# Performance work log

Hardware: AMD Instinct MI355X
Metric: run time of the kernel (lower is better)

The kernel has to match this reference:

```python
import jax, jax.numpy as jnp
import numpy as np

D, H, KVH, HD, FF = 768, 12, 4, 64, 2048
N_REP = H // KVH
EPS = 1e-6


def rmsnorm(x, w):
    # Faithful to source: norm = ||x|| * n^{-1/2}; eps added to norm (not inside sqrt)
    norm = jnp.sqrt(jnp.sum(x * x, axis=-1, keepdims=True)) * (x.shape[-1] ** -0.5)
    return w * x / (norm + EPS)


def rope_tables(seq_len, head_dim, base=10000.0):
    inv_freq = 1.0 / (base ** (np.arange(0, head_dim, 2, dtype=np.float32) / head_dim))
    t = np.arange(seq_len, dtype=np.float32)
    freqs = np.einsum('i,j->ij', t, inv_freq)  # [S, HD/2]
    emb = np.concatenate([freqs, freqs], axis=-1)  # [S, HD]
    return jnp.asarray(np.cos(emb)), jnp.asarray(np.sin(emb))


def rotate_half(x):
    h = x.shape[-1] // 2
    return jnp.concatenate([-x[..., h:], x[..., :h]], axis=-1)


def setup_inputs() -> dict:
    key = jax.random.key(0)
    ks = jax.random.split(key, 9)
    s = 0.02
    return {
        'x': jax.random.normal(ks[0], (2, 2048, D), jnp.float32),
        'Wq': jax.random.normal(ks[1], (H * HD, D), jnp.float32) * s,
        'Wk': jax.random.normal(ks[2], (KVH * HD, D), jnp.float32) * s,
        'Wv': jax.random.normal(ks[3], (KVH * HD, D), jnp.float32) * s,
        'Wo': jax.random.normal(ks[4], (D, H * HD), jnp.float32) * s,
        'Wgate': jax.random.normal(ks[5], (FF, D), jnp.float32) * s,
        'Wup': jax.random.normal(ks[6], (FF, D), jnp.float32) * s,
        'Wdown': jax.random.normal(ks[7], (D, FF), jnp.float32) * s,
        'g1': jnp.ones((D,), jnp.float32),
        'g2': jnp.ones((D,), jnp.float32),
    }


def reference(x, Wq, Wk, Wv, Wo, Wgate, Wup, Wdown, g1, g2):
    B, S, _ = x.shape
    # ---- attention sublayer (pre-norm) ----
    xn = rmsnorm(x, g1)
    q = (xn @ Wq.T).reshape(B, S, H, HD).transpose(0, 2, 1, 3)      # [B,H,S,HD]
    k = (xn @ Wk.T).reshape(B, S, KVH, HD).transpose(0, 2, 1, 3)    # [B,KVH,S,HD]
    v = (xn @ Wv.T).reshape(B, S, KVH, HD).transpose(0, 2, 1, 3)
    cos, sin = rope_tables(S, HD)                                   # [S,HD]
    q = q * cos + rotate_half(q) * sin
    k = k * cos + rotate_half(k) * sin
    # repeat kv heads to match q heads
    k = jnp.repeat(k, N_REP, axis=1)                                # [B,H,S,HD]
    v = jnp.repeat(v, N_REP, axis=1)
    scores = jnp.einsum('bhqd,bhkd->bhqk', q, k) / jnp.sqrt(jnp.float32(HD))
    causal = jnp.tril(jnp.ones((S, S), bool))
    scores = jnp.where(causal, scores, jnp.finfo(scores.dtype).min)
    attn = jax.nn.softmax(scores, axis=-1)
    out = jnp.einsum('bhqk,bhkd->bhqd', attn, v)                    # [B,H,S,HD]
    out = out.transpose(0, 2, 1, 3).reshape(B, S, H * HD) @ Wo.T
    x = x + out
    # ---- SwiGLU FFN sublayer (pre-norm) ----
    xn2 = rmsnorm(x, g2)
    ff = (jax.nn.silu(xn2 @ Wgate.T) * (xn2 @ Wup.T)) @ Wdown.T
    return x + ff
```

## Files before the change

kernel.cpp:

```cpp
#include <hip/hip_runtime.h>
#include <hip/hip_bf16.h>
#include <math.h>

typedef __bf16 bf16;
typedef __attribute__((ext_vector_type(8))) __bf16 bf16x8;
typedef __attribute__((ext_vector_type(4))) __bf16 bf16x4;
typedef __attribute__((ext_vector_type(4))) float f32x4;

#define MFMA16(a,b,c) __builtin_amdgcn_mfma_f32_16x16x32_bf16(a,b,c,0,0,0)

#define BATCH 2
#define SEQ   2048
#define DMODEL 768
#define NH    12
#define NKV   4
#define NREP  3
#define HD    64
#define FFDIM 2048
#define ROWS  (BATCH*SEQ)

#define QSCALE 0.18033688011112042f
#define LOG2E  1.4426950408889634f

#define WB(N) asm volatile("s_waitcnt vmcnt(" #N ")\n\ts_barrier" ::: "memory")
#define BAR() asm volatile("s_barrier" ::: "memory")

__device__ __forceinline__ void gl2lds16(const bf16* g, bf16* l) {
  __builtin_amdgcn_global_load_lds(
      (const __attribute__((address_space(1))) void*)g,
      (__attribute__((address_space(3))) void*)l, 16, 0, 0);
}

struct Cvt7 { const float* s[7]; bf16* d[7]; int n[7]; };
__global__ __launch_bounds__(256) void cvt_all_kernel(Cvt7 c) {
  int seg = blockIdx.y;
  const float* __restrict__ src = c.s[seg];
  bf16* __restrict__ dst = c.d[seg];
  int n4 = c.n[seg] >> 2;
  int stride = gridDim.x * 256;
  for (int i = blockIdx.x * 256 + threadIdx.x; i < n4; i += stride) {
    f32x4 v = ((const f32x4*)src)[i];
    bf16x4 o;
    #pragma unroll
    for (int j = 0; j < 4; ++j) o[j] = (bf16)v[j];
    ((bf16x4*)dst)[i] = o;
  }
}

__global__ __launch_bounds__(256) void rope_tab_kernel(float* __restrict__ tab) {
  int id = blockIdx.x * 256 + threadIdx.x;
  int j = id >> 11, s = id & 2047;
  float inv = expf(-(float)j * (9.210340371976184f / 32.0f));
  float ang = (float)s * inv;
  tab[id] = cosf(ang);
  tab[65536 + id] = sinf(ang);
}

__global__ __launch_bounds__(192) void rmsnorm_kernel(const float* __restrict__ x,
    const float* __restrict__ g, bf16* __restrict__ out) {
  int row = blockIdx.x;
  const float* xr = x + (size_t)row * DMODEL;
  int t = threadIdx.x;
  f32x4 v = *(const f32x4*)(xr + t * 4);
  float ss = v[0] * v[0] + v[1] * v[1] + v[2] * v[2] + v[3] * v[3];
  #pragma unroll
  for (int off = 32; off; off >>= 1) ss += __shfl_xor(ss, off, 64);
  __shared__ float red[3];
  if ((t & 63) == 0) red[t >> 6] = ss;
  __syncthreads();
  float total = red[0] + red[1] + red[2];
  float norm = sqrtf(total) * 0.03608439182435161f;
  float sc = 1.0f / (norm + 1e-6f);
  f32x4 gv = *(const f32x4*)(g + t * 4);
  bf16x4 o;
  #pragma unroll
  for (int i = 0; i < 4; ++i) o[i] = (bf16)(gv[i] * v[i] * sc);
  *(bf16x4*)(out + (size_t)row * DMODEL + t * 4) = o;
}

__global__ __launch_bounds__(256) void gemm_pipe64_kernel(const bf16* __restrict__ A,
    const bf16* __restrict__ B, float* __restrict__ C, const float* __restrict__ R,
    int N, int K) {
  __shared__ __align__(16) bf16 At[4][64 * 32];
  __shared__ __align__(16) bf16 Bt[4][64 * 32];
  int t = threadIdx.x, lane = t & 63, wave = t >> 6;
  int l15 = lane & 15, lq = lane >> 4;
  int wrow = (wave >> 1) * 32, wcol = (wave & 1) * 32;
  int row0 = blockIdx.y * 64, col0 = blockIdx.x * 64;
  const bf16* Ag = A + (size_t)(row0 + (t >> 2)) * K + (t & 3) * 8;
  const bf16* Bg = B + (size_t)(col0 + (t >> 2)) * K + (t & 3) * 8;
  const int NS = K / 32;

  #pragma unroll
  for (int s = 0; s < 3; ++s) {
    int ks = s * 32;
    gl2lds16(Ag + ks, At[s] + t * 8);
    gl2lds16(Bg + ks, Bt[s] + t * 8);
  }

  f32x4 zero = {0.f, 0.f, 0.f, 0.f};
  f32x4 acc[2][2];
  #pragma unroll
  for (int m = 0; m < 2; ++m)
    #pragma unroll
    for (int n = 0; n < 2; ++n) acc[m][n] = zero;

  #define GP_COMPUTE(slot) do {                                              \
    const bf16* at = At[slot]; const bf16* bt = Bt[slot];                    \
    bf16x8 af[2], bfr[2];                                                    \
    _Pragma("unroll")                                                        \
    for (int m = 0; m < 2; ++m)                                              \
      af[m] = *(const bf16x8*)(at + (wrow + m * 16 + l15) * 32 + lq * 8);    \
    _Pragma("unroll")                                                        \
    for (int n = 0; n < 2; ++n)                                              \
      bfr[n] = *(const bf16x8*)(bt + (wcol + n * 16 + l15) * 32 + lq * 8);   \
    _Pragma("unroll")                                                        \
    for (int m = 0; m < 2; ++m)                                              \
      _Pragma("unroll")                                                      \
      for (int n = 0; n < 2; ++n)                                            \
        acc[m][n] = MFMA16(af[m], bfr[n], acc[m][n]);                        \
  } while (0)

  for (int k = 0; k < NS - 3; ++k) {
    WB(4);
    int ks = (k + 3) * 32;
    gl2lds16(Ag + ks, At[(k + 3) & 3] + t * 8);
    gl2lds16(Bg + ks, Bt[(k + 3) & 3] + t * 8);
    GP_COMPUTE(k & 3);
  }
  for (int k = NS - 3; k < NS; ++k) {
    WB(0);
    GP_COMPUTE(k & 3);
  }
  #undef GP_COMPUTE

  #pragma unroll
  for (int m = 0; m < 2; ++m)
    #pragma unroll
    for (int n = 0; n < 2; ++n)
      #pragma unroll
      for (int r = 0; r < 4; ++r) {
        size_t idx = (size_t)(row0 + wrow + m * 16 + lq * 4 + r) * N
                   + (col0 + wcol + n * 16 + l15);
        C[idx] = acc[m][n][r] + R[idx];
      }
}

__global__ __launch_bounds__(256) void gemm_qkv_kernel(const bf16* __restrict__ A,
    const bf16* __restrict__ Wcat, const float* __restrict__ tab,
    bf16* __restrict__ Qh, bf16* __restrict__ Kh, bf16* __restrict__ Vt) {
  __shared__ __align__(16) bf16 At[4][64 * 32];
  __shared__ __align__(16) bf16 Bt[4][128 * 32];
  const int K = DMODEL;
  int t = threadIdx.x, lane = t & 63, wave = t >> 6;
  int l15 = lane & 15, lq = lane >> 4;
  int wrow = (wave >> 1) * 32, wcol = (wave & 1) * 64;
  int row0 = blockIdx.y * 64, col0 = blockIdx.x * 128;
  const bf16* Ag  = A + (size_t)(row0 + (t >> 2)) * K + (t & 3) * 8;
  const bf16* Bg0 = Wcat + (size_t)(col0 + (t >> 2)) * K + (t & 3) * 8;
  const bf16* Bg1 = Bg0 + (size_t)64 * K;
  const int NS = K / 32;

  #pragma unroll
  for (int s = 0; s < 3; ++s) {
    int ks = s * 32;
    gl2lds16(Ag + ks,  At[s] + t * 8);
    gl2lds16(Bg0 + ks, Bt[s] + t * 8);
    gl2lds16(Bg1 + ks, Bt[s] + 2048 + t * 8);
  }

  f32x4 zero = {0.f, 0.f, 0.f, 0.f};
  f32x4 acc[2][4];
  #pragma unroll
  for (int m = 0; m < 2; ++m)
    #pragma unroll
    for (int n = 0; n < 4; ++n) acc[m][n] = zero;

  #define QK_COMPUTE(slot) do {                                              \
    const bf16* at = At[slot]; const bf16* bt = Bt[slot];                    \
    bf16x8 af[2], bfr[4];                                                    \
    _Pragma("unroll")                                                        \
    for (int m = 0; m < 2; ++m)                                              \
      af[m] = *(const bf16x8*)(at + (wrow + m * 16 + l15) * 32 + lq * 8);    \
    _Pragma("unroll")                                                        \
    for (int n = 0; n < 4; ++n)                                              \
      bfr[n] = *(const bf16x8*)(bt + (wcol + n * 16 + l15) * 32 + lq * 8);   \
    _Pragma("unroll")                                                        \
    for (int m = 0; m < 2; ++m)                                              \
      _Pragma("unroll")                                                      \
      for (int n = 0; n < 4; ++n)                                            \
        acc[m][n] = MFMA16(af[m], bfr[n], acc[m][n]);                        \
  } while (0)

  for (int k = 0; k < NS - 3; ++k) {
    WB(6);
    int ks = (k + 3) * 32;
    gl2lds16(Ag + ks,  At[(k + 3) & 3] + t * 8);
    gl2lds16(Bg0 + ks, Bt[(k + 3) & 3] + t * 8);
    gl2lds16(Bg1 + ks, Bt[(k + 3) & 3] + 2048 + t * 8);
    QK_COMPUTE(k & 3);
  }
  for (int k = NS - 3; k < NS; ++k) {
    WB(0);
    QK_COMPUTE(k & 3);
  }
  #undef QK_COMPUTE

  int b = row0 >> 11;
  int s0 = (row0 & 2047) + wrow + lq * 4;
  int colw = col0 + wcol;
  if (colw < 768) {
    int h = colw >> 6;
    f32x4 cv[2][2], sv[2][2];
    #pragma unroll
    for (int m = 0; m < 2; ++m)
      #pragma unroll
      for (int jh = 0; jh < 2; ++jh) {
        const float* cp = tab + (jh * 16 + l15) * 2048 + s0 + m * 16;
        cv[m][jh] = *(const f32x4*)cp;
        sv[m][jh] = *(const f32x4*)(cp + 65536);
      }
    #pragma unroll
    for (int m = 0; m < 2; ++m)
      #pragma unroll
      for (int n = 0; n < 4; ++n) {
        float sgn = (n < 2) ? -1.f : 1.f;
        #pragma unroll
        for (int r = 0; r < 4; ++r) {
          float c = cv[m][n & 1][r], si = sv[m][n & 1][r];
          float rp = (acc[m][n][r] * c + sgn * acc[m][n ^ 2][r] * si) * QSCALE;
          Qh[((size_t)(b * NH + h) * SEQ + s0 + m * 16 + r) * 64 + n * 16 + l15] = (bf16)rp;
        }
      }
  } else if (colw < 1024) {
    int kh = (colw - 768) >> 6;
    f32x4 cv[2][2], sv[2][2];
    #pragma unroll
    for (int m = 0; m < 2; ++m)
      #pragma unroll
      for (int jh = 0; jh < 2; ++jh) {
        const float* cp = tab + (jh * 16 + l15) * 2048 + s0 + m * 16;
        cv[m][jh] = *(const f32x4*)cp;
        sv[m][jh] = *(const f32x4*)(cp + 65536);
      }
    #pragma unroll
    for (int m = 0; m < 2; ++m)
      #pragma unroll
      for (int n = 0; n < 4; ++n) {
        float sgn = (n < 2) ? -1.f : 1.f;
        #pragma unroll
        for (int r = 0; r < 4; ++r) {
          float c = cv[m][n & 1][r], si = sv[m][n & 1][r];
          float rp = acc[m][n][r] * c + sgn * acc[m][n ^ 2][r] * si;
          Kh[((size_t)(b * NKV + kh) * SEQ + s0 + m * 16 + r) * 64 + n * 16 + l15] = (bf16)rp;
        }
      }
  } else {
    int vh = (colw - 1024) >> 6;
    #pragma unroll
    for (int m = 0; m < 2; ++m)
      #pragma unroll
      for (int n = 0; n < 4; ++n) {
        bf16x4 pv;
        #pragma unroll
        for (int r = 0; r < 4; ++r) pv[r] = (bf16)acc[m][n][r];
        *(bf16x4*)(Vt + ((size_t)(b * NKV + vh) * 64 + n * 16 + l15) * SEQ + s0 + m * 16) = pv;
      }
  }
}

__global__ __launch_bounds__(256, 2) void gemm_gu_kernel(const bf16* __restrict__ A,
    const bf16* __restrict__ Wg, const bf16* __restrict__ Wu, bf16* __restrict__ H) {
  __shared__ __align__(16) bf16 At[3][128 * 32];
  __shared__ __align__(16) bf16 Bgt[3][128 * 32];
  __shared__ __align__(16) bf16 But[3][128 * 32];
  const int K = DMODEL;
  int t = threadIdx.x, lane = t & 63, wave = t >> 6;
  int l15 = lane & 15, lq = lane >> 4;
  int wrow = (wave >> 1) * 64, wcol = (wave & 1) * 64;
  int row0 = blockIdx.y * 128, col0 = blockIdx.x * 128;
  const bf16* Ag0 = A + (size_t)(row0 + (t >> 2)) * K + (t & 3) * 8;
  const bf16* Ag1 = Ag0 + (size_t)64 * K;
  const bf16* Gg0 = Wg + (size_t)(col0 + (t >> 2)) * K + (t & 3) * 8;
  const bf16* Gg1 = Gg0 + (size_t)64 * K;
  const bf16* Ug0 = Wu + (size_t)(col0 + (t >> 2)) * K + (t & 3) * 8;
  const bf16* Ug1 = Ug0 + (size_t)64 * K;
  const int NS = K / 32;

  #pragma unroll
  for (int s = 0; s < 2; ++s) {
    int ks = s * 32;
    gl2lds16(Ag0 + ks, At[s] + t * 8);
    gl2lds16(Ag1 + ks, At[s] + 2048 + t * 8);
    gl2lds16(Gg0 + ks, Bgt[s] + t * 8);
    gl2lds16(Gg1 + ks, Bgt[s] + 2048 + t * 8);
    gl2lds16(Ug0 + ks, But[s] + t * 8);
    gl2lds16(Ug1 + ks, But[s] + 2048 + t * 8);
  }

  f32x4 zero = {0.f, 0.f, 0.f, 0.f};
  f32x4 ag[4][4], au[4][4];
  #pragma unroll
  for (int m = 0; m < 4; ++m)
    #pragma unroll
    for (int n = 0; n < 4; ++n) { ag[m][n] = zero; au[m][n] = zero; }

  #define GU_COMPUTE(slot) do {                                              \
    const bf16* at = At[slot];                                               \
    const bf16* bgt = Bgt[slot]; const bf16* but = But[slot];                \
    bf16x8 af[4], bg[4], bu[4];                                              \
    _Pragma("unroll")                                                        \
    for (int m = 0; m < 4; ++m)                                              \
      af[m] = *(const bf16x8*)(at + (wrow + m * 16 + l15) * 32 + lq * 8);    \
    _Pragma("unroll")                                                        \
    for (int n = 0; n < 4; ++n) {                                            \
      bg[n] = *(const bf16x8*)(bgt + (wcol + n * 16 + l15) * 32 + lq * 8);   \
      bu[n] = *(const bf16x8*)(but + (wcol + n * 16 + l15) * 32 + lq * 8);   \
    }                                                                        \
    _Pragma("unroll")                                                        \
    for (int m = 0; m < 4; ++m)                                              \
      _Pragma("unroll")                                                      \
      for (int n = 0; n < 4; ++n) {                                          \
        ag[m][n] = MFMA16(af[m], bg[n], ag[m][n]);                           \
        au[m][n] = MFMA16(af[m], bu[n], au[m][n]);                           \
      }                                                                      \
  } while (0)

  int sc = 0, sw = 2;
  for (int k = 0; k < NS - 2; ++k) {
    WB(6);
    int ks = (k + 2) * 32;
    gl2lds16(Ag0 + ks, At[sw] + t * 8);
    gl2lds16(Ag1 + ks, At[sw] + 2048 + t * 8);
    gl2lds16(Gg0 + ks, Bgt[sw] + t * 8);
    gl2lds16(Gg1 + ks, Bgt[sw] + 2048 + t * 8);
    gl2lds16(Ug0 + ks, But[sw] + t * 8);
    gl2lds16(Ug1 + ks, But[sw] + 2048 + t * 8);
    GU_COMPUTE(sc);
    sc = (sc == 2) ? 0 : sc + 1;
    sw = (sw == 2) ? 0 : sw + 1;
  }
  for (int k = NS - 2; k < NS; ++k) {
    WB(0);
    GU_COMPUTE(sc);
    sc = (sc == 2) ? 0 : sc + 1;
  }
  #undef GU_COMPUTE

  #pragma unroll
  for (int m = 0; m < 4; ++m)
    #pragma unroll
    for (int n = 0; n < 4; ++n)
      #pragma unroll
      for (int r = 0; r < 4; ++r) {
        int row = row0 + wrow + m * 16 + lq * 4 + r;
        int col = col0 + wcol + n * 16 + l15;
        float g = ag[m][n][r], u = au[m][n][r];
        float sg = g / (1.f + __builtin_amdgcn_exp2f(-g * LOG2E));
        H[(size_t)row * FFDIM + col] = (bf16)(sg * u);
      }
}

__global__ __launch_bounds__(256) void attn_kernel(const bf16* __restrict__ Qh,
    const bf16* __restrict__ Kh, const bf16* __restrict__ Vt, bf16* __restrict__ out) {
  __shared__ __align__(16) bf16 Kl0[2][64 * 32];
  __shared__ __align__(16) bf16 Kl1[2][64 * 32];
  __shared__ __align__(16) bf16 Vl0[2][64 * 32];
  __shared__ __align__(16) bf16 Vl1[2][64 * 32];
  __shared__ __align__(16) bf16 P[4][16 * 80];

  int idx = blockIdx.x;
  int qt = 31 - (idx / 24);
  int bh = idx % 24;
  int q0blk = qt * 64;
  int b = bh / NH, h = bh % NH;
  int kvh = h / NREP;
  int t = threadIdx.x;
  int lane = t & 63, wave = t >> 6;
  int l15 = lane & 15, lq = lane >> 4;
  int qw = q0blk + wave * 16;
  const bf16* Qb = Qh + (size_t)(b * NH + h) * SEQ * 64;
  const bf16* Kb = Kh + (size_t)(b * NKV + kvh) * SEQ * 64;
  const bf16* Vb = Vt + (size_t)(b * NKV + kvh) * 64 * SEQ;

  bf16x8 bq0 = *(const bf16x8*)(Qb + (size_t)(qw + l15) * 64 + lq * 8);
  bf16x8 bq1 = *(const bf16x8*)(Qb + (size_t)(qw + l15) * 64 + 32 + lq * 8);

  const bf16* Kg = Kb + (size_t)(t >> 2) * 64 + (t & 3) * 8;
  const bf16* Vg = Vb + (size_t)(t >> 2) * SEQ + (t & 3) * 8;
  bf16* Pw = P[wave];
  int Pwq = l15 * 80, lq8 = lq * 8, lq4 = lq * 4;
  const int NS = qt + 1;

  #pragma unroll
  for (int s = 0; s < 2; ++s) {
    int ks = (s < NS ? s : NS - 1) * 64;
    gl2lds16(Kg + (size_t)ks * 64,      Kl0[s] + t * 8);
    gl2lds16(Kg + (size_t)ks * 64 + 32, Kl1[s] + t * 8);
    gl2lds16(Vg + ks,                   Vl0[s] + t * 8);
    gl2lds16(Vg + ks + 32,              Vl1[s] + t * 8);
  }

  f32x4 zero = {0.f, 0.f, 0.f, 0.f};
  f32x4 o[4];
  o[0] = zero; o[1] = zero; o[2] = zero; o[3] = zero;
  float l_r = 0.f;

  #define ATTN_STEP(kk, slot) do {                                           \
    int k0 = (kk) * 64;                                                      \
    const bf16* kl0 = Kl0[slot]; const bf16* kl1 = Kl1[slot];                \
    const bf16* vl0 = Vl0[slot]; const bf16* vl1 = Vl1[slot];                \
    f32x4 s[4];                                                              \
    _Pragma("unroll")                                                        \
    for (int c = 0; c < 4; ++c) {                                            \
      bf16x8 ak0 = *(const bf16x8*)(kl0 + (c * 16 + l15) * 32 + lq8);        \
      bf16x8 ak1 = *(const bf16x8*)(kl1 + (c * 16 + l15) * 32 + lq8);        \
      s[c] = zero;                                                           \
      s[c] = MFMA16(ak0, bq0, s[c]);                                         \
      s[c] = MFMA16(ak1, bq1, s[c]);                                         \
    }                                                                        \
    if (k0 + 63 > qw) {                                                      \
      int qmk = qw + l15 - k0 - lq4;                                         \
      _Pragma("unroll")                                                      \
      for (int c = 0; c < 4; ++c)                                            \
        _Pragma("unroll")                                                    \
        for (int r = 0; r < 4; ++r)                                          \
          if (c * 16 + r > qmk) s[c][r] = -INFINITY;                         \
    }                                                                        \
    _Pragma("unroll")                                                        \
    for (int c = 0; c < 4; ++c) {                                            \
      bf16x4 pe;                                                             \
      _Pragma("unroll")                                                      \
      for (int r = 0; r < 4; ++r) {                                          \
        float e = __builtin_amdgcn_exp2f(s[c][r]);                           \
        l_r += e;                                                            \
        pe[r] = (bf16)e;                                                     \
      }                                                                      \
      *(bf16x4*)(Pw + Pwq + c * 16 + lq4) = pe;                              \
    }                                                                        \
    bf16x8 bp0 = *(const bf16x8*)(Pw + Pwq + lq8);                           \
    bf16x8 bp1 = *(const bf16x8*)(Pw + Pwq + 32 + lq8);                      \
    _Pragma("unroll")                                                        \
    for (int n = 0; n < 4; ++n) {                                            \
      bf16x8 av0 = *(const bf16x8*)(vl0 + (n * 16 + l15) * 32 + lq8);        \
      bf16x8 av1 = *(const bf16x8*)(vl1 + (n * 16 + l15) * 32 + lq8);        \
      o[n] = MFMA16(av0, bp0, o[n]);                                         \
      o[n] = MFMA16(av1, bp1, o[n]);                                         \
    }                                                                        \
  } while (0)

  for (int k = 0; k < NS - 1; ++k) {
    WB(4);
    ATTN_STEP(k, k & 1);
    BAR();
    if (k <= NS - 3) {
      int ks = (k + 2) * 64;
      gl2lds16(Kg + (size_t)ks * 64,      Kl0[k & 1] + t * 8);
      gl2lds16(Kg + (size_t)ks * 64 + 32, Kl1[k & 1] + t * 8);
      gl2lds16(Vg + ks,                   Vl0[k & 1] + t * 8);
      gl2lds16(Vg + ks + 32,              Vl1[k & 1] + t * 8);
    }
  }
  {
    WB(0);
    ATTN_STEP(NS - 1, (NS - 1) & 1);
  }
  #undef ATTN_STEP

  float lt = l_r;
  lt += __shfl_xor(lt, 16, 64);
  lt += __shfl_xor(lt, 32, 64);
  float inv = 1.f / lt;
  int q = qw + l15;
  bf16* orow = out + (size_t)(b * SEQ + q) * DMODEL + h * 64;
  #pragma unroll
  for (int n = 0; n < 4; ++n) {
    bf16x4 po;
    #pragma unroll
    for (int r = 0; r < 4; ++r) po[r] = (bf16)(o[n][r] * inv);
    *(bf16x4*)(orow + n * 16 + lq4) = po;
  }
}

extern "C" void kernel_launch(void* const* d_in, const int* in_sizes, int n_in,
                              void* d_out, int out_size, void* d_ws, size_t ws_size,
                              hipStream_t stream) {
  const float* x     = (const float*)d_in[0];
  const float* Wq    = (const float*)d_in[1];
  const float* Wk    = (const float*)d_in[2];
  const float* Wv    = (const float*)d_in[3];
  const float* Wo    = (const float*)d_in[4];
  const float* Wgate = (const float*)d_in[5];
  const float* Wup   = (const float*)d_in[6];
  const float* Wdown = (const float*)d_in[7];
  const float* g1    = (const float*)d_in[8];
  const float* g2    = (const float*)d_in[9];
  float* out = (float*)d_out;

  char* ws = (char*)d_ws;
  size_t off = 0;
  auto alloc = [&](size_t bytes) { size_t o = off; off += (bytes + 255) & ~(size_t)255; return o; };
  size_t o_tab  = alloc((size_t)2 * 32 * 2048 * 4);
  size_t o_x1   = alloc((size_t)4096 * 768 * 4);
  size_t o_xn   = alloc((size_t)4096 * 768 * 2);
  size_t o_Qh   = alloc((size_t)2 * 12 * 2048 * 64 * 2);
  size_t o_Kh   = alloc((size_t)2 * 4 * 2048 * 64 * 2);
  size_t o_Vt   = alloc((size_t)2 * 4 * 64 * 2048 * 2);
  size_t o_ao   = alloc((size_t)4096 * 768 * 2);
  size_t o_H    = alloc((size_t)4096 * 2048 * 2);
  size_t o_Wcat = alloc((size_t)1280 * 768 * 2);
  size_t o_Wo   = alloc((size_t)768 * 768 * 2);
  size_t o_Wgu  = alloc((size_t)4096 * 768 * 2);
  size_t o_Wdn  = alloc((size_t)768 * 2048 * 2);
  if (ws_size < off) return;

  float* tab  = (float*)(ws + o_tab);
  float* fx1  = (float*)(ws + o_x1);
  bf16* bxn   = (bf16*)(ws + o_xn);
  bf16* bQh   = (bf16*)(ws + o_Qh);
  bf16* bKh   = (bf16*)(ws + o_Kh);
  bf16* bVt   = (bf16*)(ws + o_Vt);
  bf16* bao   = (bf16*)(ws + o_ao);
  bf16* bH    = (bf16*)(ws + o_H);
  bf16* bWcat = (bf16*)(ws + o_Wcat);
  bf16* bWo   = (bf16*)(ws + o_Wo);
  bf16* bWgu  = (bf16*)(ws + o_Wgu);
  bf16* bWdn  = (bf16*)(ws + o_Wdn);

  rope_tab_kernel<<<256, 256, 0, stream>>>(tab);

  Cvt7 c;
  c.s[0] = Wq;    c.d[0] = bWcat;              c.n[0] = 768 * 768;
  c.s[1] = Wk;    c.d[1] = bWcat + 768 * 768;  c.n[1] = 256 * 768;
  c.s[2] = Wv;    c.d[2] = bWcat + 1024 * 768; c.n[2] = 256 * 768;
  c.s[3] = Wo;    c.d[3] = bWo;                c.n[3] = 768 * 768;
  c.s[4] = Wgate; c.d[4] = bWgu;               c.n[4] = 2048 * 768;
  c.s[5] = Wup;   c.d[5] = bWgu + 2048 * 768;  c.n[5] = 2048 * 768;
  c.s[6] = Wdown; c.d[6] = bWdn;               c.n[6] = 768 * 2048;
  cvt_all_kernel<<<dim3(256, 7), 256, 0, stream>>>(c);

  rmsnorm_kernel<<<4096, 192, 0, stream>>>(x, g1, bxn);
  gemm_qkv_kernel<<<dim3(10, 64), 256, 0, stream>>>(bxn, bWcat, tab, bQh, bKh, bVt);
  attn_kernel<<<dim3(768), 256, 0, stream>>>(bQh, bKh, bVt, bao);
  gemm_pipe64_kernel<<<dim3(12, 64), 256, 0, stream>>>(bao, bWo, fx1, x, 768, 768);

  rmsnorm_kernel<<<4096, 192, 0, stream>>>(fx1, g2, bxn);
  gemm_gu_kernel<<<dim3(16, 32), 256, 0, stream>>>(bxn, bWgu, bWgu + 2048 * 768, bH);
  gemm_pipe64_kernel<<<dim3(12, 64), 256, 0, stream>>>(bH, bWdn, out, fx1, 768, 2048);
}
```

Before: 256.6 us.

## Replace triple-buffered gate/up GEMM with single-buffered 128x64 tiles

Rewrites the fused gate/up SwiGLU GEMM to use a 128x64 output tile per block (twice as many blocks) with a single LDS buffer and two barriers per K step, instead of the 128x128 tile with three-stage async prefetch. This cuts LDS and register use per block and drops the occupancy hint, aiming to raise occupancy and grid size. In exchange it gives up overlap of global loads with MFMA compute and reloads the A tile twice as often.

```diff
diff --git a/kernel.cpp b/kernel.cpp
--- a/kernel.cpp
+++ b/kernel.cpp
@@ -269,88 +269,63 @@
   }
 }
 
-__global__ __launch_bounds__(256, 2) void gemm_gu_kernel(const bf16* __restrict__ A,
+__global__ __launch_bounds__(256) void gemm_gu_kernel(const bf16* __restrict__ A,
     const bf16* __restrict__ Wg, const bf16* __restrict__ Wu, bf16* __restrict__ H) {
-  __shared__ __align__(16) bf16 At[3][128 * 32];
-  __shared__ __align__(16) bf16 Bgt[3][128 * 32];
-  __shared__ __align__(16) bf16 But[3][128 * 32];
+  __shared__ __align__(16) bf16 At[128 * 32];
+  __shared__ __align__(16) bf16 Bgt[64 * 32];
+  __shared__ __align__(16) bf16 But[64 * 32];
   const int K = DMODEL;
-  int t = threadIdx.x, lane = t & 63, wave = t >> 6;
+  int t = threadIdx.x;
+  int lane = t & 63, wave = t >> 6;
   int l15 = lane & 15, lq = lane >> 4;
-  int wrow = (wave >> 1) * 64, wcol = (wave & 1) * 64;
-  int row0 = blockIdx.y * 128, col0 = blockIdx.x * 128;
-  const bf16* Ag0 = A + (size_t)(row0 + (t >> 2)) * K + (t & 3) * 8;
+  int wrow = (wave >> 1) * 64, wcol = (wave & 1) * 32;
+  int row0 = blockIdx.y * 128;
+  int col0 = blockIdx.x * 64;
+  int srow = t >> 2, sseg = (t & 3) * 8;
+  const bf16* Ag0 = A + (size_t)(row0 + srow) * K + sseg;
   const bf16* Ag1 = Ag0 + (size_t)64 * K;
-  const bf16* Gg0 = Wg + (size_t)(col0 + (t >> 2)) * K + (t & 3) * 8;
-  const bf16* Gg1 = Gg0 + (size_t)64 * K;
-  const bf16* Ug0 = Wu + (size_t)(col0 + (t >> 2)) * K + (t & 3) * 8;
-  const bf16* Ug1 = Ug0 + (size_t)64 * K;
-  const int NS = K / 32;
-
-  #pragma unroll
-  for (int s = 0; s < 2; ++s) {
-    int ks = s * 32;
-    gl2lds16(Ag0 + ks, At[s] + t * 8);
-    gl2lds16(Ag1 + ks, At[s] + 2048 + t * 8);
-    gl2lds16(Gg0 + ks, Bgt[s] + t * 8);
-    gl2lds16(Gg1 + ks, Bgt[s] + 2048 + t * 8);
-    gl2lds16(Ug0 + ks, But[s] + t * 8);
-    gl2lds16(Ug1 + ks, But[s] + 2048 + t * 8);
-  }
+  const bf16* Gg = Wg + (size_t)(col0 + srow) * K + sseg;
+  const bf16* Ug = Wu + (size_t)(col0 + srow) * K + sseg;
+  bf16* Al0 = At + t * 8;
+  bf16* Al1 = At + 2048 + t * 8;
+  bf16* Bgd = Bgt + t * 8;
+  bf16* Bud = But + t * 8;
 
   f32x4 zero = {0.f, 0.f, 0.f, 0.f};
-  f32x4 ag[4][4], au[4][4];
+  f32x4 ag[4][2], au[4][2];
   #pragma unroll
   for (int m = 0; m < 4; ++m)
     #pragma unroll
-    for (int n = 0; n < 4; ++n) { ag[m][n] = zero; au[m][n] = zero; }
-
-  #define GU_COMPUTE(slot) do {                                              \
-    const bf16* at = At[slot];                                               \
-    const bf16* bgt = Bgt[slot]; const bf16* but = But[slot];                \
-    bf16x8 af[4], bg[4], bu[4];                                              \
-    _Pragma("unroll")                                                        \
-    for (int m = 0; m < 4; ++m)                                              \
-      af[m] = *(const bf16x8*)(at + (wrow + m * 16 + l15) * 32 + lq * 8);    \
-    _Pragma("unroll")                                                        \
-    for (int n = 0; n < 4; ++n) {                                            \
-      bg[n] = *(const bf16x8*)(bgt + (wcol + n * 16 + l15) * 32 + lq * 8);   \
-      bu[n] = *(const bf16x8*)(but + (wcol + n * 16 + l15) * 32 + lq * 8);   \
-    }                                                                        \
-    _Pragma("unroll")                                                        \
-    for (int m = 0; m < 4; ++m)                                              \
-      _Pragma("unroll")                                                      \
-      for (int n = 0; n < 4; ++n) {                                          \
-        ag[m][n] = MFMA16(af[m], bg[n], ag[m][n]);                           \
-        au[m][n] = MFMA16(af[m], bu[n], au[m][n]);                           \
-      }                                                                      \
-  } while (0)
-
-  int sc = 0, sw = 2;
-  for (int k = 0; k < NS - 2; ++k) {
-    WB(6);
-    int ks = (k + 2) * 32;
-    gl2lds16(Ag0 + ks, At[sw] + t * 8);
-    gl2lds16(Ag1 + ks, At[sw] + 2048 + t * 8);
-    gl2lds16(Gg0 + ks, Bgt[sw] + t * 8);
-    gl2lds16(Gg1 + ks, Bgt[sw] + 2048 + t * 8);
-    gl2lds16(Ug0 + ks, But[sw] + t * 8);
-    gl2lds16(Ug1 + ks, But[sw] + 2048 + t * 8);
-    GU_COMPUTE(sc);
-    sc = (sc == 2) ? 0 : sc + 1;
-    sw = (sw == 2) ? 0 : sw + 1;
-  }
-  for (int k = NS - 2; k < NS; ++k) {
-    WB(0);
-    GU_COMPUTE(sc);
-    sc = (sc == 2) ? 0 : sc + 1;
-  }
-  #undef GU_COMPUTE
-
+    for (int n = 0; n < 2; ++n) { ag[m][n] = zero; au[m][n] = zero; }
+
+  for (int k0 = 0; k0 < K; k0 += 32) {
+    __syncthreads();
+    gl2lds16(Ag0 + k0, Al0);
+    gl2lds16(Ag1 + k0, Al1);
+    gl2lds16(Gg + k0, Bgd);
+    gl2lds16(Ug + k0, Bud);
+    __syncthreads();
+    bf16x8 af[4], bg[2], bu[2];
+    #pragma unroll
+    for (int m = 0; m < 4; ++m)
+      af[m] = *(const bf16x8*)(At + (wrow + m * 16 + l15) * 32 + lq * 8);
+    #pragma unroll
+    for (int n = 0; n < 2; ++n) {
+      bg[n] = *(const bf16x8*)(Bgt + (wcol + n * 16 + l15) * 32 + lq * 8);
+      bu[n] = *(const bf16x8*)(But + (wcol + n * 16 + l15) * 32 + lq * 8);
+    }
+    #pragma unroll
+    for (int m = 0; m < 4; ++m)
+      #pragma unroll
+      for (int n = 0; n < 2; ++n) {
+        ag[m][n] = MFMA16(af[m], bg[n], ag[m][n]);
+        au[m][n] = MFMA16(af[m], bu[n], au[m][n]);
+      }
+  }
   #pragma unroll
   for (int m = 0; m < 4; ++m)
     #pragma unroll
-    for (int n = 0; n < 4; ++n)
+    for (int n = 0; n < 2; ++n)
       #pragma unroll
       for (int r = 0; r < 4; ++r) {
         int row = row0 + wrow + m * 16 + lq * 4 + r;
@@ -545,6 +520,6 @@
   gemm_pipe64_kernel<<<dim3(12, 64), 256, 0, stream>>>(bao, bWo, fx1, x, 768, 768);
 
   rmsnorm_kernel<<<4096, 192, 0, stream>>>(fx1, g2, bxn);
-  gemm_gu_kernel<<<dim3(16, 32), 256, 0, stream>>>(bxn, bWgu, bWgu + 2048 * 768, bH);
+  gemm_gu_kernel<<<dim3(32, 32), 256, 0, stream>>>(bxn, bWgu, bWgu + 2048 * 768, bH);
   gemm_pipe64_kernel<<<dim3(12, 64), 256, 0, stream>>>(bH, bWdn, out, fx1, 768, 2048);
 }
```

After: 259.9 us. Within noise of the previous version (+1.3%).
